# Kernel tuning notes

Measured on AMD Instinct MI355X. Metric: run time of the kernel, lower is better.

Reference implementation:

```python
import jax, jax.numpy as jnp
import numpy as np

N_NODES = 50000
N_EDGES = 500000
NODE_DIM = 128
EDGE_DIM = 128
HIDDEN = 256


def setup_inputs() -> dict:
    key = jax.random.key(0)
    k1, k2, k3, k4, k5 = jax.random.split(key, 5)
    node_features = jax.random.normal(k1, (N_NODES, NODE_DIM), dtype=jnp.float32)
    edge_features = jax.random.normal(k2, (N_EDGES, EDGE_DIM), dtype=jnp.float32)
    edge_index = jax.random.randint(k3, (2, N_EDGES), 0, N_NODES, dtype=jnp.int64)
    in_dim = 2 * NODE_DIM + EDGE_DIM
    W1 = jax.random.normal(k4, (in_dim, HIDDEN), dtype=jnp.float32) * (1.0 / np.sqrt(in_dim))
    b1 = jnp.zeros((HIDDEN,), dtype=jnp.float32)
    W2 = jax.random.normal(k5, (HIDDEN, EDGE_DIM), dtype=jnp.float32) * (1.0 / np.sqrt(HIDDEN))
    b2 = jnp.zeros((EDGE_DIM,), dtype=jnp.float32)
    return {"node_features": node_features, "edge_features": edge_features,
            "edge_index": edge_index, "W1": W1, "b1": b1, "W2": W2, "b2": b2}


def reference(node_features, edge_features, edge_index, W1, b1, W2, b2):
    # h_edge' = h_edge + MLP(concat(h_src, h_dst, h_edge)); dropout is identity (eval)
    src, dst = edge_index[0], edge_index[1]
    h_src = node_features[src]                    # (E, node_dim)
    h_dst = node_features[dst]                    # (E, node_dim)
    combined = jnp.concatenate([h_src, h_dst, edge_features], axis=1)  # (E, 2*nd+ed)
    h = jax.nn.relu(combined @ W1 + b1)           # (E, hidden)
    update = h @ W2 + b2                          # (E, edge_dim)
    return edge_features + update
```

## Files before the change

### kernel.cpp

```cpp
#include <hip/hip_runtime.h>

#define E_TOTAL   500000
#define NN        50000
#define ND        128
#define ED        128
#define HID       256
#define IND       384
#define EB        64
#define NBLOCKS   ((E_TOTAL + EB - 1) / EB)

typedef float  f32x4  __attribute__((ext_vector_type(4)));
typedef short  bf16x8 __attribute__((ext_vector_type(8)));

__device__ __forceinline__ unsigned short f2bf(float f) {
    unsigned int u = __float_as_uint(f);
    u += 0x7FFFu + ((u >> 16) & 1u);
    return (unsigned short)(u >> 16);
}
__device__ __forceinline__ float bf2f(unsigned short h) {
    return __uint_as_float(((unsigned int)h) << 16);
}

__global__ void prep_weights(const float* __restrict__ w1, const float* __restrict__ w2,
                             unsigned short* __restrict__ w1t, unsigned short* __restrict__ w2t) {
    int i = blockIdx.x * blockDim.x + threadIdx.x;
    if (i < IND * HID) {
        int k = i / HID, n = i % HID;
        w1t[n * IND + k] = f2bf(w1[i]);
    } else if (i < IND * HID + HID * ED) {
        int q = i - IND * HID;
        int k = q / ED, n = q % ED;
        w2t[n * HID + k] = f2bf(w2[q]);
    }
}

__global__ __launch_bounds__(256, 2)
void prep_ptab(const float* __restrict__ nf,
               const unsigned short* __restrict__ w1t,
               const float* __restrict__ b1,
               unsigned short* __restrict__ Psrc,
               unsigned short* __restrict__ Pdst) {
    __shared__ unsigned short An[64 * ND];
    const int tid  = threadIdx.x;
    const int base = blockIdx.x * 64;
    const int lane = tid & 63;
    const int w    = tid >> 6;
    const int l15  = lane & 15;
    const int lhi  = lane >> 4;

    #pragma unroll
    for (int it = 0; it < 4; ++it) {
        int item = tid + it * 256;
        int row = item >> 4, cc = item & 15;
        int nidx = base + row;
        if (nidx >= NN) nidx = NN - 1;
        const float* p = nf + (size_t)nidx * ND + cc * 8;
        float4 f0 = *(const float4*)p;
        float4 f1 = *(const float4*)(p + 4);
        bf16x8 val;
        val[0] = (short)f2bf(f0.x); val[1] = (short)f2bf(f0.y);
        val[2] = (short)f2bf(f0.z); val[3] = (short)f2bf(f0.w);
        val[4] = (short)f2bf(f1.x); val[5] = (short)f2bf(f1.y);
        val[6] = (short)f2bf(f1.z); val[7] = (short)f2bf(f1.w);
        *(bf16x8*)(An + row * ND + ((cc * 8) ^ ((row & 7) * 8))) = val;
    }
    __syncthreads();

    f32x4 accs[4][4], accd[4][4];
    #pragma unroll
    for (int mt = 0; mt < 4; ++mt)
        #pragma unroll
        for (int nt = 0; nt < 4; ++nt) { accs[mt][nt] = (f32x4)0.0f; accd[mt][nt] = (f32x4)0.0f; }

    #pragma unroll
    for (int ks = 0; ks < 4; ++ks) {
        int c0 = ks * 32 + lhi * 8;
        bf16x8 a[4];
        #pragma unroll
        for (int mt = 0; mt < 4; ++mt) {
            int row = mt * 16 + l15;
            a[mt] = *(const bf16x8*)(An + row * ND + (c0 ^ ((row & 7) * 8)));
        }
        #pragma unroll
        for (int nt = 0; nt < 4; ++nt) {
            int n = w * 64 + nt * 16 + l15;
            bf16x8 bs = *(const bf16x8*)(w1t + (size_t)n * IND + c0);
            bf16x8 bd = *(const bf16x8*)(w1t + (size_t)n * IND + 128 + c0);
            #pragma unroll
            for (int mt = 0; mt < 4; ++mt) {
                accs[mt][nt] = __builtin_amdgcn_mfma_f32_16x16x32_bf16(a[mt], bs, accs[mt][nt], 0, 0, 0);
                accd[mt][nt] = __builtin_amdgcn_mfma_f32_16x16x32_bf16(a[mt], bd, accd[mt][nt], 0, 0, 0);
            }
        }
    }

    #pragma unroll
    for (int nt = 0; nt < 4; ++nt) {
        int col = w * 64 + nt * 16 + l15;
        float bias = b1[col];
        #pragma unroll
        for (int mt = 0; mt < 4; ++mt) {
            #pragma unroll
            for (int r = 0; r < 4; ++r) {
                int row = mt * 16 + lhi * 4 + r;
                int nidx = base + row;
                if (nidx < NN) {
                    size_t off = (size_t)nidx * HID + col;
                    Psrc[off] = f2bf(accs[mt][nt][r] + bias);
                    Pdst[off] = f2bf(accd[mt][nt][r]);
                }
            }
        }
    }
}

__global__ __launch_bounds__(256, 3)
void edge_mlp(const float* __restrict__ edgef,
              const int* __restrict__ eidx,
              const unsigned short* __restrict__ Psrc,
              const unsigned short* __restrict__ Pdst,
              const unsigned short* __restrict__ w1t,
              const unsigned short* __restrict__ w2t,
              const float* __restrict__ b2,
              float* __restrict__ out) {
    __shared__ unsigned short Ae[EB * ND];
    __shared__ unsigned short Hs[EB * HID];

    const int tid  = threadIdx.x;
    const int base = blockIdx.x * EB;
    const int lane = tid & 63;
    const int w    = tid >> 6;
    const int l15  = lane & 15;
    const int lhi  = lane >> 4;
    const int* srcI = eidx;
    const int* dstI = eidx + E_TOTAL;

    {
        bf16x8 vs[8], vd[8];
        float4 e0[4], e1[4];

        #pragma unroll
        for (int it = 0; it < 8; ++it) {
            int item = tid + it * 256;
            int row = item >> 5, cc = item & 31;
            int e = base + row;
            int el = e < E_TOTAL ? e : E_TOTAL - 1;
            int s = srcI[el], d = dstI[el];
            vs[it] = *(const bf16x8*)(Psrc + (size_t)s * HID + cc * 8);
            vd[it] = *(const bf16x8*)(Pdst + (size_t)d * HID + cc * 8);
        }
        #pragma unroll
        for (int it = 0; it < 4; ++it) {
            int item = tid + it * 256;
            int row = item >> 4, cc = item & 15;
            int e = base + row;
            int el = e < E_TOTAL ? e : E_TOTAL - 1;
            const float* p = edgef + (size_t)el * ED + cc * 8;
            e0[it] = *(const float4*)p;
            e1[it] = *(const float4*)(p + 4);
        }

        #pragma unroll
        for (int it = 0; it < 8; ++it) {
            int item = tid + it * 256;
            int row = item >> 5, cc = item & 31;
            bf16x8 o;
            #pragma unroll
            for (int j = 0; j < 8; ++j)
                o[j] = (short)f2bf(bf2f((unsigned short)vs[it][j]) + bf2f((unsigned short)vd[it][j]));
            *(bf16x8*)(Hs + row * HID + ((cc * 8) ^ ((row & 7) * 8))) = o;
        }
        #pragma unroll
        for (int it = 0; it < 4; ++it) {
            int item = tid + it * 256;
            int row = item >> 4, cc = item & 15;
            bf16x8 val;
            val[0] = (short)f2bf(e0[it].x); val[1] = (short)f2bf(e0[it].y);
            val[2] = (short)f2bf(e0[it].z); val[3] = (short)f2bf(e0[it].w);
            val[4] = (short)f2bf(e1[it].x); val[5] = (short)f2bf(e1[it].y);
            val[6] = (short)f2bf(e1[it].z); val[7] = (short)f2bf(e1[it].w);
            *(bf16x8*)(Ae + row * ND + ((cc * 8) ^ ((row & 7) * 8))) = val;
        }
    }
    __syncthreads();

    f32x4 acc1[4][4];
    #pragma unroll
    for (int mt = 0; mt < 4; ++mt)
        #pragma unroll
        for (int nt = 0; nt < 4; ++nt)
            acc1[mt][nt] = (f32x4)0.0f;

    #pragma unroll
    for (int ks = 0; ks < 4; ++ks) {
        int c0 = ks * 32 + lhi * 8;
        bf16x8 a[4];
        #pragma unroll
        for (int mt = 0; mt < 4; ++mt) {
            int row = mt * 16 + l15;
            a[mt] = *(const bf16x8*)(Ae + row * ND + (c0 ^ ((row & 7) * 8)));
        }
        #pragma unroll
        for (int nt = 0; nt < 4; ++nt) {
            int n = w * 64 + nt * 16 + l15;
            bf16x8 b = *(const bf16x8*)(w1t + (size_t)n * IND + 256 + c0);
            #pragma unroll
            for (int mt = 0; mt < 4; ++mt)
                acc1[mt][nt] = __builtin_amdgcn_mfma_f32_16x16x32_bf16(a[mt], b, acc1[mt][nt], 0, 0, 0);
        }
    }

    #pragma unroll
    for (int nt = 0; nt < 4; ++nt) {
        int col = w * 64 + nt * 16 + l15;
        #pragma unroll
        for (int mt = 0; mt < 4; ++mt) {
            #pragma unroll
            for (int r = 0; r < 4; ++r) {
                int row = mt * 16 + lhi * 4 + r;
                int idx = row * HID + (col ^ ((row & 7) * 8));
                float v = acc1[mt][nt][r] + bf2f(Hs[idx]);
                v = v > 0.0f ? v : 0.0f;
                Hs[idx] = f2bf(v);
            }
        }
    }
    __syncthreads();

    f32x4 acc2[4][2];
    #pragma unroll
    for (int mt = 0; mt < 4; ++mt)
        #pragma unroll
        for (int nt = 0; nt < 2; ++nt)
            acc2[mt][nt] = (f32x4)0.0f;

    #pragma unroll
    for (int ks = 0; ks < 8; ++ks) {
        int c0 = ks * 32 + lhi * 8;
        bf16x8 a[4];
        #pragma unroll
        for (int mt = 0; mt < 4; ++mt) {
            int row = mt * 16 + l15;
            a[mt] = *(const bf16x8*)(Hs + row * HID + (c0 ^ ((row & 7) * 8)));
        }
        #pragma unroll
        for (int nt = 0; nt < 2; ++nt) {
            int n = w * 32 + nt * 16 + l15;
            bf16x8 b = *(const bf16x8*)(w2t + (size_t)n * HID + c0);
            #pragma unroll
            for (int mt = 0; mt < 4; ++mt)
                acc2[mt][nt] = __builtin_amdgcn_mfma_f32_16x16x32_bf16(a[mt], b, acc2[mt][nt], 0, 0, 0);
        }
    }

    #pragma unroll
    for (int nt = 0; nt < 2; ++nt) {
        int col = w * 32 + nt * 16 + l15;
        float bias = b2[col];
        #pragma unroll
        for (int mt = 0; mt < 4; ++mt) {
            #pragma unroll
            for (int r = 0; r < 4; ++r) {
                int row = mt * 16 + lhi * 4 + r;
                int e = base + row;
                if (e < E_TOTAL) {
                    float ev = bf2f(Ae[row * ND + (col ^ ((row & 7) * 8))]);
                    out[(size_t)e * ED + col] = ev + acc2[mt][nt][r] + bias;
                }
            }
        }
    }
}

extern "C" void kernel_launch(void* const* d_in, const int* in_sizes, int n_in,
                              void* d_out, int out_size, void* d_ws, size_t ws_size,
                              hipStream_t stream) {
    const float* nf   = (const float*)d_in[0];
    const float* ef   = (const float*)d_in[1];
    const int*   eidx = (const int*)d_in[2];
    const float* W1   = (const float*)d_in[3];
    const float* b1   = (const float*)d_in[4];
    const float* W2   = (const float*)d_in[5];
    const float* b2   = (const float*)d_in[6];
    float* out = (float*)d_out;

    unsigned short* w1t  = (unsigned short*)d_ws;
    unsigned short* w2t  = w1t + IND * HID;
    unsigned short* Psrc = w2t + HID * ED;
    unsigned short* Pdst = Psrc + (size_t)NN * HID;

    int wtotal = IND * HID + HID * ED;
    prep_weights<<<(wtotal + 255) / 256, 256, 0, stream>>>(W1, W2, w1t, w2t);
    prep_ptab<<<(NN + 63) / 64, 256, 0, stream>>>(nf, w1t, b1, Psrc, Pdst);
    edge_mlp<<<NBLOCKS, 256, 0, stream>>>(ef, eidx, Psrc, Pdst, w1t, w2t, b2, out);
}
```

Baseline: 299.7 us.

## Shrink edge tile to 48 rows, raise occupancy, use packed bf16 convert

Reduces the per-block edge tile from 64 to 48 rows, cutting LDS and register use, and raises launch bounds to 4 blocks per SIMD-group so more blocks can be resident to hide gather latency. It replaces software round-to-nearest bf16 conversion with the hardware v_cvt_pk_bf16_f32 instruction, converting pairs of floats at once. It also splits the gather and edge-feature loads into separate scopes to lower live register pressure. The smaller tile raises the block count and reloads weight fragments more often per edge.

Measured after the change: 328.4 us. 1.1x slower.

```diff
diff --git a/kernel.cpp b/kernel.cpp
--- a/kernel.cpp
+++ b/kernel.cpp
@@ -6,11 +6,12 @@
 #define ED        128
 #define HID       256
 #define IND       384
-#define EB        64
+#define EB        48
 #define NBLOCKS   ((E_TOTAL + EB - 1) / EB)
 
 typedef float  f32x4  __attribute__((ext_vector_type(4)));
 typedef short  bf16x8 __attribute__((ext_vector_type(8)));
+typedef unsigned int u32x4 __attribute__((ext_vector_type(4)));
 
 __device__ __forceinline__ unsigned short f2bf(float f) {
     unsigned int u = __float_as_uint(f);
@@ -19,6 +20,11 @@
 }
 __device__ __forceinline__ float bf2f(unsigned short h) {
     return __uint_as_float(((unsigned int)h) << 16);
+}
+__device__ __forceinline__ unsigned int cvtpk(float lo, float hi) {
+    unsigned int r;
+    asm("v_cvt_pk_bf16_f32 %0, %1, %2" : "=v"(r) : "v"(lo), "v"(hi));
+    return r;
 }
 
 __global__ void prep_weights(const float* __restrict__ w1, const float* __restrict__ w2,
@@ -26,11 +32,11 @@
     int i = blockIdx.x * blockDim.x + threadIdx.x;
     if (i < IND * HID) {
         int k = i / HID, n = i % HID;
-        w1t[n * IND + k] = f2bf(w1[i]);
+        w1t[n * IND + k] = (unsigned short)cvtpk(w1[i], 0.f);
     } else if (i < IND * HID + HID * ED) {
         int q = i - IND * HID;
         int k = q / ED, n = q % ED;
-        w2t[n * HID + k] = f2bf(w2[q]);
+        w2t[n * HID + k] = (unsigned short)cvtpk(w2[q], 0.f);
     }
 }
 
@@ -57,12 +63,10 @@
         const float* p = nf + (size_t)nidx * ND + cc * 8;
         float4 f0 = *(const float4*)p;
         float4 f1 = *(const float4*)(p + 4);
-        bf16x8 val;
-        val[0] = (short)f2bf(f0.x); val[1] = (short)f2bf(f0.y);
-        val[2] = (short)f2bf(f0.z); val[3] = (short)f2bf(f0.w);
-        val[4] = (short)f2bf(f1.x); val[5] = (short)f2bf(f1.y);
-        val[6] = (short)f2bf(f1.z); val[7] = (short)f2bf(f1.w);
-        *(bf16x8*)(An + row * ND + ((cc * 8) ^ ((row & 7) * 8))) = val;
+        u32x4 val;
+        val[0] = cvtpk(f0.x, f0.y); val[1] = cvtpk(f0.z, f0.w);
+        val[2] = cvtpk(f1.x, f1.y); val[3] = cvtpk(f1.z, f1.w);
+        *(u32x4*)(An + row * ND + ((cc * 8) ^ ((row & 7) * 8))) = val;
     }
     __syncthreads();
 
@@ -106,15 +110,15 @@
                 int nidx = base + row;
                 if (nidx < NN) {
                     size_t off = (size_t)nidx * HID + col;
-                    Psrc[off] = f2bf(accs[mt][nt][r] + bias);
-                    Pdst[off] = f2bf(accd[mt][nt][r]);
+                    Psrc[off] = (unsigned short)cvtpk(accs[mt][nt][r] + bias, 0.f);
+                    Pdst[off] = (unsigned short)cvtpk(accd[mt][nt][r], 0.f);
                 }
             }
         }
     }
 }
 
-__global__ __launch_bounds__(256, 3)
+__global__ __launch_bounds__(256, 4)
 void edge_mlp(const float* __restrict__ edgef,
               const int* __restrict__ eidx,
               const unsigned short* __restrict__ Psrc,
@@ -136,11 +140,9 @@
     const int* dstI = eidx + E_TOTAL;
 
     {
-        bf16x8 vs[8], vd[8];
-        float4 e0[4], e1[4];
-
-        #pragma unroll
-        for (int it = 0; it < 8; ++it) {
+        bf16x8 vs[6], vd[6];
+        #pragma unroll
+        for (int it = 0; it < 6; ++it) {
             int item = tid + it * 256;
             int row = item >> 5, cc = item & 31;
             int e = base + row;
@@ -150,7 +152,23 @@
             vd[it] = *(const bf16x8*)(Pdst + (size_t)d * HID + cc * 8);
         }
         #pragma unroll
-        for (int it = 0; it < 4; ++it) {
+        for (int it = 0; it < 6; ++it) {
+            int item = tid + it * 256;
+            int row = item >> 5, cc = item & 31;
+            u32x4 o;
+            #pragma unroll
+            for (int jj = 0; jj < 4; ++jj) {
+                float a0 = bf2f((unsigned short)vs[it][2*jj])   + bf2f((unsigned short)vd[it][2*jj]);
+                float a1 = bf2f((unsigned short)vs[it][2*jj+1]) + bf2f((unsigned short)vd[it][2*jj+1]);
+                o[jj] = cvtpk(a0, a1);
+            }
+            *(u32x4*)(Hs + row * HID + ((cc * 8) ^ ((row & 7) * 8))) = o;
+        }
+    }
+    {
+        float4 e0[3], e1[3];
+        #pragma unroll
+        for (int it = 0; it < 3; ++it) {
             int item = tid + it * 256;
             int row = item >> 4, cc = item & 15;
             int e = base + row;
@@ -159,34 +177,21 @@
             e0[it] = *(const float4*)p;
             e1[it] = *(const float4*)(p + 4);
         }
-
-        #pragma unroll
-        for (int it = 0; it < 8; ++it) {
-            int item = tid + it * 256;
-            int row = item >> 5, cc = item & 31;
-            bf16x8 o;
-            #pragma unroll
-            for (int j = 0; j < 8; ++j)
-                o[j] = (short)f2bf(bf2f((unsigned short)vs[it][j]) + bf2f((unsigned short)vd[it][j]));
-            *(bf16x8*)(Hs + row * HID + ((cc * 8) ^ ((row & 7) * 8))) = o;
-        }
-        #pragma unroll
-        for (int it = 0; it < 4; ++it) {
+        #pragma unroll
+        for (int it = 0; it < 3; ++it) {
             int item = tid + it * 256;
             int row = item >> 4, cc = item & 15;
-            bf16x8 val;
-            val[0] = (short)f2bf(e0[it].x); val[1] = (short)f2bf(e0[it].y);
-            val[2] = (short)f2bf(e0[it].z); val[3] = (short)f2bf(e0[it].w);
-            val[4] = (short)f2bf(e1[it].x); val[5] = (short)f2bf(e1[it].y);
-            val[6] = (short)f2bf(e1[it].z); val[7] = (short)f2bf(e1[it].w);
-            *(bf16x8*)(Ae + row * ND + ((cc * 8) ^ ((row & 7) * 8))) = val;
+            u32x4 val;
+            val[0] = cvtpk(e0[it].x, e0[it].y); val[1] = cvtpk(e0[it].z, e0[it].w);
+            val[2] = cvtpk(e1[it].x, e1[it].y); val[3] = cvtpk(e1[it].z, e1[it].w);
+            *(u32x4*)(Ae + row * ND + ((cc * 8) ^ ((row & 7) * 8))) = val;
         }
     }
     __syncthreads();
 
-    f32x4 acc1[4][4];
-    #pragma unroll
-    for (int mt = 0; mt < 4; ++mt)
+    f32x4 acc1[3][4];
+    #pragma unroll
+    for (int mt = 0; mt < 3; ++mt)
         #pragma unroll
         for (int nt = 0; nt < 4; ++nt)
             acc1[mt][nt] = (f32x4)0.0f;
@@ -194,9 +199,9 @@
     #pragma unroll
     for (int ks = 0; ks < 4; ++ks) {
         int c0 = ks * 32 + lhi * 8;
-        bf16x8 a[4];
-        #pragma unroll
-        for (int mt = 0; mt < 4; ++mt) {
+        bf16x8 a[3];
+        #pragma unroll
+        for (int mt = 0; mt < 3; ++mt) {
             int row = mt * 16 + l15;
             a[mt] = *(const bf16x8*)(Ae + row * ND + (c0 ^ ((row & 7) * 8)));
         }
@@ -205,7 +210,7 @@
             int n = w * 64 + nt * 16 + l15;
             bf16x8 b = *(const bf16x8*)(w1t + (size_t)n * IND + 256 + c0);
             #pragma unroll
-            for (int mt = 0; mt < 4; ++mt)
+            for (int mt = 0; mt < 3; ++mt)
                 acc1[mt][nt] = __builtin_amdgcn_mfma_f32_16x16x32_bf16(a[mt], b, acc1[mt][nt], 0, 0, 0);
         }
     }
@@ -214,22 +219,22 @@
     for (int nt = 0; nt < 4; ++nt) {
         int col = w * 64 + nt * 16 + l15;
         #pragma unroll
-        for (int mt = 0; mt < 4; ++mt) {
+        for (int mt = 0; mt < 3; ++mt) {
             #pragma unroll
             for (int r = 0; r < 4; ++r) {
                 int row = mt * 16 + lhi * 4 + r;
                 int idx = row * HID + (col ^ ((row & 7) * 8));
                 float v = acc1[mt][nt][r] + bf2f(Hs[idx]);
                 v = v > 0.0f ? v : 0.0f;
-                Hs[idx] = f2bf(v);
+                Hs[idx] = (unsigned short)cvtpk(v, 0.f);
             }
         }
     }
     __syncthreads();
 
-    f32x4 acc2[4][2];
-    #pragma unroll
-    for (int mt = 0; mt < 4; ++mt)
+    f32x4 acc2[3][2];
+    #pragma unroll
+    for (int mt = 0; mt < 3; ++mt)
         #pragma unroll
         for (int nt = 0; nt < 2; ++nt)
             acc2[mt][nt] = (f32x4)0.0f;
@@ -237,9 +242,9 @@
     #pragma unroll
     for (int ks = 0; ks < 8; ++ks) {
         int c0 = ks * 32 + lhi * 8;
-        bf16x8 a[4];
-        #pragma unroll
-        for (int mt = 0; mt < 4; ++mt) {
+        bf16x8 a[3];
+        #pragma unroll
+        for (int mt = 0; mt < 3; ++mt) {
             int row = mt * 16 + l15;
             a[mt] = *(const bf16x8*)(Hs + row * HID + (c0 ^ ((row & 7) * 8)));
         }
@@ -248,7 +253,7 @@
             int n = w * 32 + nt * 16 + l15;
             bf16x8 b = *(const bf16x8*)(w2t + (size_t)n * HID + c0);
             #pragma unroll
-            for (int mt = 0; mt < 4; ++mt)
+            for (int mt = 0; mt < 3; ++mt)
                 acc2[mt][nt] = __builtin_amdgcn_mfma_f32_16x16x32_bf16(a[mt], b, acc2[mt][nt], 0, 0, 0);
         }
     }
@@ -258,7 +263,7 @@
         int col = w * 32 + nt * 16 + l15;
         float bias = b2[col];
         #pragma unroll
-        for (int mt = 0; mt < 4; ++mt) {
+        for (int mt = 0; mt < 3; ++mt) {
             #pragma unroll
             for (int r = 0; r < 4; ++r) {
                 int row = mt * 16 + lhi * 4 + r;
```
